# Kernel tuning notes

Measured on AMD Instinct MI355X. Metric: run time of the kernel, lower is better.

The kernel has to match this reference:

```python
import jax, jax.numpy as jnp
import numpy as np

E = 8        # num_experts
K = 2        # experts_per_token
D = 1024     # embed_dim
F = 4096     # expert intermediate (mlp_ratio * D)
FS = 2048    # shared-expert intermediate (n_shared_experts * D)
B, S = 2, 1024


def setup_inputs() -> dict:
    key = jax.random.key(0)
    ks = jax.random.split(key, 8)
    scale = jnp.float32(0.02)
    return {
        "x": jax.random.normal(ks[0], (B, S, D), jnp.float32),
        "gate_w": jax.random.normal(ks[1], (E, D), jnp.float32) * scale,
        "gate_k": jax.random.normal(ks[2], (E, D, F), jnp.float32) * scale,
        "up_k": jax.random.normal(ks[3], (E, D, F), jnp.float32) * scale,
        "down_k": jax.random.normal(ks[4], (E, F, D), jnp.float32) * scale,
        "sh_gate": jax.random.normal(ks[5], (D, FS), jnp.float32) * scale,
        "sh_up": jax.random.normal(ks[6], (D, FS), jnp.float32) * scale,
        "sh_down": jax.random.normal(ks[7], (FS, D), jnp.float32) * scale,
    }


def reference(x, gate_w, gate_k, up_k, down_k, sh_gate, sh_up, sh_down):
    b, s, d = x.shape
    xt = x.reshape(-1, d)                                   # [N, D] tokens

    # --- router gate: softmax over expert logits, then top-k ---
    logits = xt @ gate_w.T                                  # [N, E]
    scores = jax.nn.softmax(logits, axis=-1)
    topk_w, topk_i = jax.lax.top_k(scores, K)               # [N, K] each
    # norm_topk_prob = False -> use raw softmax top-k weights

    # per-token combine weights over experts: [N, E]
    combine = (jax.nn.one_hot(topk_i, E, dtype=xt.dtype) * topk_w[..., None]).sum(axis=1)

    # --- routed experts: SwiGLU MLP per expert (batched over E) ---
    g = jnp.einsum("nd,edf->enf", xt, gate_k)               # [E, N, F]
    u = jnp.einsum("nd,edf->enf", xt, up_k)                 # [E, N, F]
    a = jax.nn.silu(g) * u                                  # [E, N, F]
    eo = jnp.einsum("enf,efd->end", a, down_k)              # [E, N, D]
    y = jnp.einsum("end,ne->nd", eo, combine)               # [N, D]

    # --- shared expert (SwiGLU) on identity input ---
    shared = (jax.nn.silu(xt @ sh_gate) * (xt @ sh_up)) @ sh_down  # [N, D]

    return (y + shared).reshape(b, s, d)
```

## Files before the change

### kernel.cpp

```cpp
#include <hip/hip_runtime.h>
#include <hip/hip_bf16.h>

#define E_ 8
#define K_ 2
#define D_ 1024
#define F_ 4096
#define FS_ 2048
#define N_ 2048
#define ROWS_CAP 4352
#define NCHUNK 8
#define CHUNK_CAP 8

typedef __bf16 bf16x8 __attribute__((ext_vector_type(8)));
typedef float f32x4 __attribute__((ext_vector_type(4)));

static __device__ __forceinline__ unsigned short f2bf(float f) {
  union { float f; unsigned int u; } v; v.f = f;
  unsigned int u = v.u;
  return (unsigned short)((u + 0x7FFF + ((u >> 16) & 1)) >> 16);
}

static __device__ __forceinline__ void gload16(const unsigned short* gp, unsigned short* lp) {
  __builtin_amdgcn_global_load_lds(
      (const __attribute__((address_space(1))) unsigned int*)gp,
      (__attribute__((address_space(3))) unsigned int*)lp, 16, 0, 0);
}

__global__ void init_k(int* counts) {
  if (threadIdx.x < E_) counts[threadIdx.x] = 0;
}

__global__ void router_k(const float* __restrict__ x, const float* __restrict__ gw,
                         unsigned short* __restrict__ xbf, float* __restrict__ topw,
                         int* __restrict__ topi, int* __restrict__ counts) {
  int wave = threadIdx.x >> 6, lane = threadIdx.x & 63;
  int n = blockIdx.x * 4 + wave;
  const float* xr = x + (size_t)n * D_;
  float v[16];
#pragma unroll
  for (int j = 0; j < 16; ++j) v[j] = xr[lane + 64 * j];
#pragma unroll
  for (int j = 0; j < 16; ++j) xbf[(size_t)n * D_ + lane + 64 * j] = f2bf(v[j]);
  float logit[E_];
  for (int e = 0; e < E_; ++e) {
    const float* g = gw + e * D_;
    float acc = 0.f;
#pragma unroll
    for (int j = 0; j < 16; ++j) acc += v[j] * g[lane + 64 * j];
#pragma unroll
    for (int off = 32; off > 0; off >>= 1) acc += __shfl_down(acc, off, 64);
    logit[e] = __shfl(acc, 0, 64);
  }
  if (lane == 0) {
    float m = logit[0];
    for (int e = 1; e < E_; ++e) m = fmaxf(m, logit[e]);
    float p[E_], s = 0.f;
    for (int e = 0; e < E_; ++e) { p[e] = expf(logit[e] - m); s += p[e]; }
    float inv = 1.f / s;
    for (int e = 0; e < E_; ++e) p[e] *= inv;
    int i0 = 0;
    for (int e = 1; e < E_; ++e) if (p[e] > p[i0]) i0 = e;
    int i1 = (i0 == 0) ? 1 : 0;
    for (int e = 0; e < E_; ++e) if (e != i0 && p[e] > p[i1]) i1 = e;
    topi[n * 2] = i0; topi[n * 2 + 1] = i1;
    topw[n * 2] = p[i0]; topw[n * 2 + 1] = p[i1];
    atomicAdd(&counts[i0], 1);
    atomicAdd(&counts[i1], 1);
  }
}

__global__ void scan_k(const int* __restrict__ counts, int* __restrict__ offs,
                       int* __restrict__ cursor, int* __restrict__ tile_e,
                       int* __restrict__ tile_m) {
  if (threadIdx.x == 0) {
    int load[NCHUNK];
    for (int c = 0; c < NCHUNK; ++c) load[c] = 0;
    for (int i = 0; i < NCHUNK * CHUNK_CAP; ++i) tile_e[i] = -1;
    int o = 0;
    for (int e = 0; e < E_; ++e) {
      offs[e] = o;
      int c = counts[e];
      int mt = (c + 127) >> 7;
      int best = 0;
      for (int c2 = 1; c2 < NCHUNK; ++c2) if (load[c2] < load[best]) best = c2;
      for (int m = 0; m < mt; ++m) {
        int ch = best;
        if (load[ch] >= CHUNK_CAP) {
          ch = 0;
          for (int c2 = 1; c2 < NCHUNK; ++c2) if (load[c2] < load[ch]) ch = c2;
        }
        tile_e[ch * CHUNK_CAP + load[ch]] = e;
        tile_m[ch * CHUNK_CAP + load[ch]] = m;
        load[ch]++;
      }
      o += c; cursor[e] = 0;
    }
    offs[E_] = o;
  }
}

__global__ void fill_k(const int* __restrict__ topi, const float* __restrict__ topw,
                       const int* __restrict__ offs,
                       int* __restrict__ cursor, int* __restrict__ rowlist,
                       int* __restrict__ slot_of, float* __restrict__ roww) {
  int n = blockIdx.x * blockDim.x + threadIdx.x;
  if (n >= N_) return;
  for (int k = 0; k < K_; ++k) {
    int e = topi[n * 2 + k];
    int pos = offs[e] + atomicAdd(&cursor[e], 1);
    rowlist[pos] = n;
    slot_of[n * 2 + k] = pos;
    roww[pos] = topw[n * 2 + k];
  }
}

__global__ void transpose_cvt_k(const float* __restrict__ in, unsigned short* __restrict__ out,
                                int R, int C) {
  __shared__ float tile[64][65];
  int cb = blockIdx.x * 64, rb = blockIdx.y * 64;
  const float* ip = in + (size_t)blockIdx.z * R * C;
  unsigned short* op = out + (size_t)blockIdx.z * R * C;
  int t = threadIdx.x;
  int cg = (t & 15) * 4, r0 = t >> 4;
#pragma unroll
  for (int p = 0; p < 4; ++p) {
    int r = r0 + p * 16;
    float4 v = *(const float4*)&ip[(size_t)(rb + r) * C + cb + cg];
    tile[r][cg] = v.x; tile[r][cg + 1] = v.y; tile[r][cg + 2] = v.z; tile[r][cg + 3] = v.w;
  }
  __syncthreads();
  int wx = t & 31, wy = t >> 5;
#pragma unroll
  for (int i = 0; i < 8; ++i) {
    int cl = wy + i * 8;
    unsigned int u = (unsigned int)f2bf(tile[2 * wx][cl]) |
                     ((unsigned int)f2bf(tile[2 * wx + 1][cl]) << 16);
    ((unsigned int*)(op + (size_t)(cb + cl) * R + rb))[wx] = u;
  }
}

#define G1_STAGE(buf, kt2)                               \
    gload16(aptr0 + (kt2) * 32, &As[buf][aoff0]);        \
    gload16(aptr1 + (kt2) * 32, &As[buf][aoff1]);        \
    gload16(bgptr + (kt2) * 32, &Bgs[buf][boff]);        \
    gload16(buptr + (kt2) * 32, &Bus[buf][boff]);

#define G1_STEP(buf, kt)                                                        \
  {                                                                             \
    if ((kt) + 1 < nk) {                                                        \
      G1_STAGE(1 - (buf), (kt) + 1)                                             \
      asm volatile("s_waitcnt vmcnt(4)" ::: "memory");                          \
    } else {                                                                    \
      asm volatile("s_waitcnt vmcnt(0)" ::: "memory");                          \
    }                                                                           \
    __builtin_amdgcn_s_barrier();                                               \
    __builtin_amdgcn_sched_barrier(0);                                          \
    bf16x8 afr[4];                                                              \
    _Pragma("unroll") for (int i = 0; i < 4; ++i)                               \
      afr[i] = *(const bf16x8*)&As[buf][(wm * 64 + i * 16 + (lane & 15)) * 32 + (lane >> 4) * 8]; \
    _Pragma("unroll") for (int j = 0; j < 2; ++j) {                             \
      bf16x8 bg = *(const bf16x8*)&Bgs[buf][(wn * 32 + j * 16 + (lane & 15)) * 32 + (lane >> 4) * 8]; \
      bf16x8 bu = *(const bf16x8*)&Bus[buf][(wn * 32 + j * 16 + (lane & 15)) * 32 + (lane >> 4) * 8]; \
      _Pragma("unroll") for (int i = 0; i < 4; ++i) {                           \
        accg[i][j] = __builtin_amdgcn_mfma_f32_16x16x32_bf16(afr[i], bg, accg[i][j], 0, 0, 0); \
        accu[i][j] = __builtin_amdgcn_mfma_f32_16x16x32_bf16(afr[i], bu, accu[i][j], 0, 0, 0); \
      }                                                                         \
    }                                                                           \
    __builtin_amdgcn_sched_barrier(0);                                          \
    __builtin_amdgcn_s_barrier();                                               \
  }

__launch_bounds__(256, 3)
__global__ void gemm1_k(const unsigned short* __restrict__ Abase,
                        const int* __restrict__ rowlist,
                        const int* __restrict__ offs,
                        const int* __restrict__ tile_e, const int* __restrict__ tile_m,
                        int swz, int Mfixed,
                        const unsigned short* __restrict__ Bg_base,
                        const unsigned short* __restrict__ Bu_base,
                        int Ncols, int Kdim,
                        unsigned short* __restrict__ Out) {
  int e, mbase, Me, slotbase, nbase;
  if (swz) {
    int slot = blockIdx.x * CHUNK_CAP + (blockIdx.y & (CHUNK_CAP - 1));
    e = tile_e[slot];
    if (e < 0) return;
    mbase = tile_m[slot] * 128;
    slotbase = offs[e]; Me = offs[e + 1] - slotbase;
    nbase = (int)(blockIdx.y >> 3) * 64;
  } else {
    e = 0; mbase = blockIdx.x * 128; slotbase = 0; Me = Mfixed;
    nbase = blockIdx.y * 64;
  }
  const unsigned short* Bg = Bg_base + (size_t)e * Ncols * Kdim;
  const unsigned short* Bu = Bu_base + (size_t)e * Ncols * Kdim;

  __shared__ unsigned short As[2][128 * 32];
  __shared__ unsigned short Bgs[2][64 * 32];
  __shared__ unsigned short Bus[2][64 * 32];

  int t = threadIdx.x, lane = t & 63, wave = t >> 6;
  int wm = wave >> 1, wn = wave & 1;
  int chunk = lane & 3, rsub = lane >> 2;

  int g0 = mbase + wave * 32 + rsub;
  int g1 = mbase + wave * 32 + 16 + rsub;
  int src0, src1;
  if (rowlist) {
    src0 = rowlist[slotbase + ((g0 < Me) ? (g0 - mbase) + mbase : 0)];
    src1 = rowlist[slotbase + ((g1 < Me) ? g1 : 0)];
    src0 = rowlist[slotbase + ((g0 < Me) ? g0 : 0)];
  } else {
    src0 = (g0 < Me) ? g0 : 0;
    src1 = (g1 < Me) ? g1 : 0;
  }
  const unsigned short* aptr0 = Abase + (size_t)src0 * Kdim + chunk * 8;
  const unsigned short* aptr1 = Abase + (size_t)src1 * Kdim + chunk * 8;
  unsigned int aoff0 = (unsigned)(wave * 32) * 32;
  unsigned int aoff1 = (unsigned)(wave * 32 + 16) * 32;
  int bn = nbase + wave * 16 + rsub;
  const unsigned short* bgptr = Bg + (size_t)bn * Kdim + chunk * 8;
  const unsigned short* buptr = Bu + (size_t)bn * Kdim + chunk * 8;
  unsigned int boff = (unsigned)(wave * 16) * 32;

  f32x4 accg[4][2], accu[4][2];
#pragma unroll
  for (int i = 0; i < 4; ++i)
#pragma unroll
    for (int j = 0; j < 2; ++j) {
      accg[i][j] = f32x4{0.f, 0.f, 0.f, 0.f};
      accu[i][j] = f32x4{0.f, 0.f, 0.f, 0.f};
    }

  int nk = Kdim >> 5;
  G1_STAGE(0, 0)
  for (int kt = 0; kt < nk; kt += 2) {
    G1_STEP(0, kt)
    G1_STEP(1, kt + 1)
  }

  int r0 = (lane >> 4) * 4, cn = lane & 15;
#pragma unroll
  for (int i = 0; i < 4; ++i) {
#pragma unroll
    for (int rr = 0; rr < 4; ++rr) {
      int grow = mbase + wm * 64 + i * 16 + r0 + rr;
      if (grow < Me) {
        size_t rbase = (size_t)(slotbase + grow) * Ncols + nbase;
#pragma unroll
        for (int j = 0; j < 2; ++j) {
          float g = accg[i][j][rr], u = accu[i][j][rr];
          float a = (g / (1.f + __expf(-g))) * u;
          Out[rbase + wn * 32 + j * 16 + cn] = f2bf(a);
        }
      }
    }
  }
}

#define G2_STAGE(buf, kt2)                               \
    gload16(aptr0 + (kt2) * 32, &As[buf][loff0]);        \
    gload16(aptr1 + (kt2) * 32, &As[buf][loff1]);        \
    gload16(bptr0 + (kt2) * 32, &Bs[buf][loff0]);        \
    gload16(bptr1 + (kt2) * 32, &Bs[buf][loff1]);

#define G2_STEP(buf, kt)                                                        \
  {                                                                             \
    if ((kt) + 1 < nk) {                                                        \
      G2_STAGE(1 - (buf), (kt) + 1)                                             \
      asm volatile("s_waitcnt vmcnt(4)" ::: "memory");                          \
    } else {                                                                    \
      asm volatile("s_waitcnt vmcnt(0)" ::: "memory");                          \
    }                                                                           \
    __builtin_amdgcn_s_barrier();                                               \
    __builtin_amdgcn_sched_barrier(0);                                          \
    bf16x8 afr[4];                                                              \
    _Pragma("unroll") for (int i = 0; i < 4; ++i)                               \
      afr[i] = *(const bf16x8*)&As[buf][(wm * 64 + i * 16 + (lane & 15)) * 32 + (lane >> 4) * 8]; \
    _Pragma("unroll") for (int j = 0; j < 4; ++j) {                             \
      bf16x8 bb = *(const bf16x8*)&Bs[buf][(wn * 64 + j * 16 + (lane & 15)) * 32 + (lane >> 4) * 8]; \
      _Pragma("unroll") for (int i = 0; i < 4; ++i)                             \
        acc[i][j] = __builtin_amdgcn_mfma_f32_16x16x32_bf16(afr[i], bb, acc[i][j], 0, 0, 0); \
    }                                                                           \
    __builtin_amdgcn_sched_barrier(0);                                          \
    __builtin_amdgcn_s_barrier();                                               \
  }

__launch_bounds__(256, 3)
__global__ void gemm2_k(const unsigned short* __restrict__ Abase,
                        const int* __restrict__ rowlist,
                        const float* __restrict__ roww,
                        const int* __restrict__ offs,
                        const int* __restrict__ tile_e, const int* __restrict__ tile_m,
                        int swz, int Mfixed,
                        const unsigned short* __restrict__ Bt_base,
                        int Ncols, int Kdim, int kchunk,
                        float* __restrict__ Out) {
  int e, mbase, Me, slotbase, nbase, koff;
  if (swz) {
    int slot = blockIdx.x * CHUNK_CAP + (blockIdx.y & (CHUNK_CAP - 1));
    e = tile_e[slot];
    if (e < 0) return;
    mbase = tile_m[slot] * 128;
    slotbase = offs[e]; Me = offs[e + 1] - slotbase;
    int r = blockIdx.y >> 3;
    nbase = (r & 7) * 128;
    koff = (r >> 3) * kchunk;
  } else {
    e = 0; mbase = blockIdx.x * 128; slotbase = 0; Me = Mfixed;
    nbase = blockIdx.y * 128;
    koff = blockIdx.z * kchunk;
  }
  const unsigned short* Bt = Bt_base + (size_t)e * Ncols * Kdim;

  __shared__ unsigned short As[2][128 * 32];
  __shared__ unsigned short Bs[2][128 * 32];

  int t = threadIdx.x, lane = t & 63, wave = t >> 6;
  int wm = wave >> 1, wn = wave & 1;
  int chunk = lane & 3, rsub = lane >> 2;

  int ra = wave * 32 + rsub, rb2 = wave * 32 + 16 + rsub;
  int g0 = mbase + ra, g1 = mbase + rb2;
  int arow0 = slotbase + ((g0 < Me) ? g0 : 0);
  int arow1 = slotbase + ((g1 < Me) ? g1 : 0);
  const unsigned short* aptr0 = Abase + (size_t)arow0 * Kdim + koff + chunk * 8;
  const unsigned short* aptr1 = Abase + (size_t)arow1 * Kdim + koff + chunk * 8;
  const unsigned short* bptr0 = Bt + (size_t)(nbase + ra) * Kdim + koff + chunk * 8;
  const unsigned short* bptr1 = Bt + (size_t)(nbase + rb2) * Kdim + koff + chunk * 8;
  unsigned int loff0 = (unsigned)(wave * 32) * 32;
  unsigned int loff1 = (unsigned)(wave * 32 + 16) * 32;

  f32x4 acc[4][4];
#pragma unroll
  for (int i = 0; i < 4; ++i)
#pragma unroll
    for (int j = 0; j < 4; ++j) acc[i][j] = f32x4{0.f, 0.f, 0.f, 0.f};

  int nk = kchunk >> 5;
  G2_STAGE(0, 0)
  for (int kt = 0; kt < nk; kt += 2) {
    G2_STEP(0, kt)
    G2_STEP(1, kt + 1)
  }

  int er0 = (lane >> 4) * 4, cn = lane & 15;
#pragma unroll
  for (int i = 0; i < 4; ++i) {
#pragma unroll
    for (int rr = 0; rr < 4; ++rr) {
      int grow = mbase + wm * 64 + i * 16 + er0 + rr;
      if (grow < Me) {
        int srow = slotbase + grow;
        int token; float wgt;
        if (rowlist) { token = rowlist[srow]; wgt = roww[srow]; }
        else { token = grow; wgt = 1.f; }
        float* orow = Out + (size_t)token * Ncols + nbase + wn * 64 + cn;
#pragma unroll
        for (int j = 0; j < 4; ++j)
          atomicAdd(&orow[j * 16], wgt * acc[i][j][rr]);
      }
    }
  }
}

__launch_bounds__(256, 2)
__global__ void gemm1_old(const unsigned short* __restrict__ Abase,
                          const int* __restrict__ rowlist,
                          const int* __restrict__ offs, int Mfixed,
                          const float* __restrict__ Bg_base,
                          const float* __restrict__ Bu_base,
                          int Ncols, int Kdim,
                          unsigned short* __restrict__ Out) {
  int e = blockIdx.z;
  int Me, slotbase;
  if (offs) { slotbase = offs[e]; Me = offs[e + 1] - slotbase; }
  else      { slotbase = 0;       Me = Mfixed; }
  int mbase = blockIdx.x * 128;
  if (mbase >= Me) return;
  int nbase = blockIdx.y * 128;
  const float* Bg = Bg_base + (size_t)e * Kdim * Ncols;
  const float* Bu = Bu_base + (size_t)e * Kdim * Ncols;
  __shared__ unsigned short As[128][40];
  __shared__ unsigned short Bgs[128][40];
  __shared__ unsigned short Bus[128][40];
  int t = threadIdx.x, lane = t & 63, wave = t >> 6;
  int wm = wave >> 1, wn = wave & 1;
  f32x4 accg[4][4], accu[4][4];
#pragma unroll
  for (int i = 0; i < 4; ++i)
#pragma unroll
    for (int j = 0; j < 4; ++j) {
      accg[i][j] = f32x4{0.f, 0.f, 0.f, 0.f};
      accu[i][j] = f32x4{0.f, 0.f, 0.f, 0.f};
    }
  int ar = t >> 1, akh = t & 1;
  int arow = mbase + ar;
  int asrc = 0;
  if (arow < Me) asrc = rowlist ? rowlist[slotbase + arow] : arow;
  const unsigned short* aptr = Abase + (size_t)asrc * Kdim + akh * 16;
  int bfc = t & 127, bkh = t >> 7;
  const float* bgp = Bg + (size_t)(bkh * 16) * Ncols + nbase + bfc;
  const float* bup = Bu + (size_t)(bkh * 16) * Ncols + nbase + bfc;
  int nk = Kdim >> 5;
  for (int kt = 0; kt < nk; ++kt) {
    uint4 a0 = *(const uint4*)(aptr + kt * 32);
    uint4 a1 = *(const uint4*)(aptr + kt * 32 + 8);
    *(uint4*)&As[ar][akh * 16] = a0;
    *(uint4*)&As[ar][akh * 16 + 8] = a1;
    {
      const float* p0 = bgp + (size_t)kt * 32 * Ncols;
      float bv[16]; unsigned short h[16];
#pragma unroll
      for (int i = 0; i < 16; ++i) bv[i] = p0[(size_t)i * Ncols];
#pragma unroll
      for (int i = 0; i < 16; ++i) h[i] = f2bf(bv[i]);
      *(uint4*)&Bgs[bfc][bkh * 16] = *(uint4*)&h[0];
      *(uint4*)&Bgs[bfc][bkh * 16 + 8] = *(uint4*)&h[8];
    }
    {
      const float* p1 = bup + (size_t)kt * 32 * Ncols;
      float bv[16]; unsigned short h[16];
#pragma unroll
      for (int i = 0; i < 16; ++i) bv[i] = p1[(size_t)i * Ncols];
#pragma unroll
      for (int i = 0; i < 16; ++i) h[i] = f2bf(bv[i]);
      *(uint4*)&Bus[bfc][bkh * 16] = *(uint4*)&h[0];
      *(uint4*)&Bus[bfc][bkh * 16 + 8] = *(uint4*)&h[8];
    }
    __syncthreads();
    bf16x8 afr[4];
#pragma unroll
    for (int i = 0; i < 4; ++i)
      afr[i] = *(const bf16x8*)&As[wm * 64 + i * 16 + (lane & 15)][(lane >> 4) * 8];
#pragma unroll
    for (int j = 0; j < 4; ++j) {
      bf16x8 bg = *(const bf16x8*)&Bgs[wn * 64 + j * 16 + (lane & 15)][(lane >> 4) * 8];
      bf16x8 bu = *(const bf16x8*)&Bus[wn * 64 + j * 16 + (lane & 15)][(lane >> 4) * 8];
#pragma unroll
      for (int i = 0; i < 4; ++i) {
        accg[i][j] = __builtin_amdgcn_mfma_f32_16x16x32_bf16(afr[i], bg, accg[i][j], 0, 0, 0);
        accu[i][j] = __builtin_amdgcn_mfma_f32_16x16x32_bf16(afr[i], bu, accu[i][j], 0, 0, 0);
      }
    }
    __syncthreads();
  }
  int r0 = (lane >> 4) * 4, cn = lane & 15;
#pragma unroll
  for (int i = 0; i < 4; ++i) {
#pragma unroll
    for (int rr = 0; rr < 4; ++rr) {
      int grow = mbase + wm * 64 + i * 16 + r0 + rr;
      if (grow < Me) {
        size_t rbase = (size_t)(slotbase + grow) * Ncols + nbase;
#pragma unroll
        for (int j = 0; j < 4; ++j) {
          float g = accg[i][j][rr], u = accu[i][j][rr];
          float a = (g / (1.f + __expf(-g))) * u;
          Out[rbase + wn * 64 + j * 16 + cn] = f2bf(a);
        }
      }
    }
  }
}

__launch_bounds__(256, 2)
__global__ void gemm2_old(const unsigned short* __restrict__ Abase,
                          const int* __restrict__ offs, int Mfixed,
                          const float* __restrict__ B_base,
                          int Ncols, int Kdim,
                          float* __restrict__ Out) {
  int e = blockIdx.z;
  int Me, slotbase;
  if (offs) { slotbase = offs[e]; Me = offs[e + 1] - slotbase; }
  else      { slotbase = 0;       Me = Mfixed; }
  int mbase = blockIdx.x * 128;
  if (mbase >= Me) return;
  int nbase = blockIdx.y * 128;
  const float* B = B_base + (size_t)e * Kdim * Ncols;
  __shared__ unsigned short As[128][40];
  __shared__ unsigned short Bs[128][40];
  int t = threadIdx.x, lane = t & 63, wave = t >> 6;
  int wm = wave >> 1, wn = wave & 1;
  f32x4 acc[4][4];
#pragma unroll
  for (int i = 0; i < 4; ++i)
#pragma unroll
    for (int j = 0; j < 4; ++j) acc[i][j] = f32x4{0.f, 0.f, 0.f, 0.f};
  int ar = t >> 1, akh = t & 1;
  int arow = slotbase + ((mbase + ar < Me) ? (mbase + ar) : 0);
  const unsigned short* aptr = Abase + (size_t)arow * Kdim + akh * 16;
  int bfc = t & 127, bkh = t >> 7;
  const float* bp = B + (size_t)(bkh * 16) * Ncols + nbase + bfc;
  int nk = Kdim >> 5;
  for (int kt = 0; kt < nk; ++kt) {
    uint4 a0 = *(const uint4*)(aptr + kt * 32);
    uint4 a1 = *(const uint4*)(aptr + kt * 32 + 8);
    *(uint4*)&As[ar][akh * 16] = a0;
    *(uint4*)&As[ar][akh * 16 + 8] = a1;
    {
      const float* p0 = bp + (size_t)kt * 32 * Ncols;
      float bv[16]; unsigned short h[16];
#pragma unroll
      for (int i = 0; i < 16; ++i) bv[i] = p0[(size_t)i * Ncols];
#pragma unroll
      for (int i = 0; i < 16; ++i) h[i] = f2bf(bv[i]);
      *(uint4*)&Bs[bfc][bkh * 16] = *(uint4*)&h[0];
      *(uint4*)&Bs[bfc][bkh * 16 + 8] = *(uint4*)&h[8];
    }
    __syncthreads();
    bf16x8 afr[4];
#pragma unroll
    for (int i = 0; i < 4; ++i)
      afr[i] = *(const bf16x8*)&As[wm * 64 + i * 16 + (lane & 15)][(lane >> 4) * 8];
#pragma unroll
    for (int j = 0; j < 4; ++j) {
      bf16x8 bb = *(const bf16x8*)&Bs[wn * 64 + j * 16 + (lane & 15)][(lane >> 4) * 8];
#pragma unroll
      for (int i = 0; i < 4; ++i)
        acc[i][j] = __builtin_amdgcn_mfma_f32_16x16x32_bf16(afr[i], bb, acc[i][j], 0, 0, 0);
    }
    __syncthreads();
  }
  int r0 = (lane >> 4) * 4, cn = lane & 15;
#pragma unroll
  for (int i = 0; i < 4; ++i) {
#pragma unroll
    for (int rr = 0; rr < 4; ++rr) {
      int grow = mbase + wm * 64 + i * 16 + r0 + rr;
      if (grow < Me) {
        size_t rbase = (size_t)(slotbase + grow) * Ncols + nbase;
#pragma unroll
        for (int j = 0; j < 4; ++j)
          Out[rbase + wn * 64 + j * 16 + cn] = acc[i][j][rr];
      }
    }
  }
}

__global__ void combine_k(const float* __restrict__ eo, const float* __restrict__ sh,
                          const float* __restrict__ topw, const int* __restrict__ slot_of,
                          float* __restrict__ out) {
  int idx = blockIdx.x * blockDim.x + threadIdx.x;
  int n = idx >> 8;
  int d4 = idx & 255;
  float w0 = topw[n * 2], w1 = topw[n * 2 + 1];
  int s0 = slot_of[n * 2], s1 = slot_of[n * 2 + 1];
  float4 a = ((const float4*)(eo + (size_t)s0 * D_))[d4];
  float4 b = ((const float4*)(eo + (size_t)s1 * D_))[d4];
  float4 c = ((const float4*)(sh + (size_t)n * D_))[d4];
  float4 r;
  r.x = w0 * a.x + w1 * b.x + c.x;
  r.y = w0 * a.y + w1 * b.y + c.y;
  r.z = w0 * a.z + w1 * b.z + c.z;
  r.w = w0 * a.w + w1 * b.w + c.w;
  ((float4*)out)[idx] = r;
}

extern "C" void kernel_launch(void* const* d_in, const int* in_sizes, int n_in,
                              void* d_out, int out_size, void* d_ws, size_t ws_size,
                              hipStream_t stream) {
  const float* x  = (const float*)d_in[0];
  const float* gw = (const float*)d_in[1];
  const float* gk = (const float*)d_in[2];
  const float* uk = (const float*)d_in[3];
  const float* dk = (const float*)d_in[4];
  const float* sg = (const float*)d_in[5];
  const float* su = (const float*)d_in[6];
  const float* sd = (const float*)d_in[7];
  float* out = (float*)d_out;

  char* w = (char*)d_ws;
  size_t o = 0;
  auto take = [&](size_t bytes) -> void* {
    void* p = w + o;
    o += (bytes + 255) & ~(size_t)255;
    return p;
  };
  unsigned short* xbf    = (unsigned short*)take((size_t)N_ * D_ * 2);
  unsigned short* act    = (unsigned short*)take((size_t)ROWS_CAP * F_ * 2);
  unsigned short* act_sh = (unsigned short*)take((size_t)N_ * FS_ * 2);
  float* eo     = (float*)take((size_t)ROWS_CAP * D_ * 4);
  float* sh_out = (float*)take((size_t)N_ * D_ * 4);
  float* topw   = (float*)take((size_t)N_ * 2 * 4);
  int* topi     = (int*)take((size_t)N_ * 2 * 4);
  int* slot_of  = (int*)take((size_t)N_ * 2 * 4);
  int* rowlist  = (int*)take((size_t)ROWS_CAP * 4);
  int* counts   = (int*)take(E_ * 4);
  int* offs     = (int*)take((E_ + 1) * 4);
  int* cursor   = (int*)take(E_ * 4);
  int* tile_e   = (int*)take(NCHUNK * CHUNK_CAP * 4);
  int* tile_m   = (int*)take(NCHUNK * CHUNK_CAP * 4);
  float* roww = eo;
  unsigned short* gkt = (unsigned short*)take((size_t)E_ * D_ * F_ * 2);
  unsigned short* ukt = (unsigned short*)take((size_t)E_ * D_ * F_ * 2);
  unsigned short* dkt = (unsigned short*)take((size_t)E_ * D_ * F_ * 2);
  unsigned short* sgt = (unsigned short*)take((size_t)D_ * FS_ * 2);
  unsigned short* sut = (unsigned short*)take((size_t)D_ * FS_ * 2);
  unsigned short* sdt = (unsigned short*)take((size_t)D_ * FS_ * 2);
  bool full = (ws_size >= o);

  hipLaunchKernelGGL(init_k, dim3(1), dim3(64), 0, stream, counts);
  hipLaunchKernelGGL(router_k, dim3(N_ / 4), dim3(256), 0, stream,
                     x, gw, xbf, topw, topi, counts);
  hipLaunchKernelGGL(scan_k, dim3(1), dim3(32), 0, stream,
                     counts, offs, cursor, tile_e, tile_m);
  hipLaunchKernelGGL(fill_k, dim3(N_ / 256), dim3(256), 0, stream,
                     topi, topw, offs, cursor, rowlist, slot_of, roww);

  if (full) {
    hipLaunchKernelGGL(transpose_cvt_k, dim3(F_ / 64, D_ / 64, E_), dim3(256), 0, stream,
                       gk, gkt, D_, F_);
    hipLaunchKernelGGL(transpose_cvt_k, dim3(F_ / 64, D_ / 64, E_), dim3(256), 0, stream,
                       uk, ukt, D_, F_);
    hipLaunchKernelGGL(transpose_cvt_k, dim3(D_ / 64, F_ / 64, E_), dim3(256), 0, stream,
                       dk, dkt, F_, D_);
    hipLaunchKernelGGL(transpose_cvt_k, dim3(FS_ / 64, D_ / 64, 1), dim3(256), 0, stream,
                       sg, sgt, D_, FS_);
    hipLaunchKernelGGL(transpose_cvt_k, dim3(FS_ / 64, D_ / 64, 1), dim3(256), 0, stream,
                       su, sut, D_, FS_);
    hipLaunchKernelGGL(transpose_cvt_k, dim3(D_ / 64, FS_ / 64, 1), dim3(256), 0, stream,
                       sd, sdt, FS_, D_);
    hipMemsetAsync(out, 0, (size_t)N_ * D_ * 4, stream);
    hipLaunchKernelGGL(gemm1_k, dim3(NCHUNK, CHUNK_CAP * (F_ / 64)), dim3(256), 0, stream,
                       xbf, rowlist, offs, tile_e, tile_m, 1, 0,
                       gkt, ukt, F_, D_, act);
    hipLaunchKernelGGL(gemm1_k, dim3(N_ / 128, FS_ / 64), dim3(256), 0, stream,
                       xbf, (const int*)nullptr, (const int*)nullptr,
                       (const int*)nullptr, (const int*)nullptr, 0, N_,
                       sgt, sut, FS_, D_, act_sh);
    hipLaunchKernelGGL(gemm2_k, dim3(NCHUNK, CHUNK_CAP * (D_ / 128) * 2), dim3(256), 0, stream,
                       act, rowlist, roww, offs, tile_e, tile_m, 1, 0,
                       dkt, D_, F_, F_ / 2, out);
    hipLaunchKernelGGL(gemm2_k, dim3(N_ / 128, D_ / 128, 2), dim3(256), 0, stream,
                       act_sh, (const int*)nullptr, (const float*)nullptr,
                       (const int*)nullptr, (const int*)nullptr, (const int*)nullptr, 0, N_,
                       sdt, D_, FS_, FS_ / 2, out);
  } else {
    hipLaunchKernelGGL(gemm1_old, dim3(16, F_ / 128, E_), dim3(256), 0, stream,
                       xbf, rowlist, offs, 0, gk, uk, F_, D_, act);
    hipLaunchKernelGGL(gemm1_old, dim3(16, FS_ / 128, 1), dim3(256), 0, stream,
                       xbf, (const int*)nullptr, (const int*)nullptr, N_, sg, su, FS_, D_, act_sh);
    hipLaunchKernelGGL(gemm2_old, dim3(16, D_ / 128, E_), dim3(256), 0, stream,
                       act, offs, 0, dk, D_, F_, eo);
    hipLaunchKernelGGL(gemm2_old, dim3(16, D_ / 128, 1), dim3(256), 0, stream,
                       act_sh, (const int*)nullptr, N_, sd, D_, FS_, sh_out);
    hipLaunchKernelGGL(combine_k, dim3((N_ * D_ / 4) / 256), dim3(256), 0, stream,
                       eo, sh_out, topw, slot_of, out);
  }
}
```

Measured before the change: 794.9 us.

## Use chunk-major LDS tile layout and simplify double-buffer synchronization in MoE GEMMs

Both grouped GEMM kernels change their LDS tile layout so each 16-row slab is stored chunk-major. The lanes of an MFMA operand read then hit contiguous LDS addresses, which removes the strided row accesses that caused bank conflicts. The hand-written vmcnt waits and split barriers are replaced by a prefetch-next, compute-current, __syncthreads loop, and a redundant rowlist load is removed. The trade-off is that each barrier now waits for the prefetch just issued, which may reduce how much of the global-load latency is hidden.

```diff
diff --git a/kernel.cpp b/kernel.cpp
--- a/kernel.cpp
+++ b/kernel.cpp
@@ -145,29 +145,19 @@
     gload16(bgptr + (kt2) * 32, &Bgs[buf][boff]);        \
     gload16(buptr + (kt2) * 32, &Bus[buf][boff]);
 
-#define G1_STEP(buf, kt)                                                        \
+#define G1_COMPUTE(buf)                                                         \
   {                                                                             \
-    if ((kt) + 1 < nk) {                                                        \
-      G1_STAGE(1 - (buf), (kt) + 1)                                             \
-      asm volatile("s_waitcnt vmcnt(4)" ::: "memory");                          \
-    } else {                                                                    \
-      asm volatile("s_waitcnt vmcnt(0)" ::: "memory");                          \
-    }                                                                           \
-    __builtin_amdgcn_s_barrier();                                               \
-    __builtin_amdgcn_sched_barrier(0);                                          \
     bf16x8 afr[4];                                                              \
     _Pragma("unroll") for (int i = 0; i < 4; ++i)                               \
-      afr[i] = *(const bf16x8*)&As[buf][(wm * 64 + i * 16 + (lane & 15)) * 32 + (lane >> 4) * 8]; \
+      afr[i] = *(const bf16x8*)&As[buf][(wm * 4 + i) * 512 + chunk * 128 + rsub * 8]; \
     _Pragma("unroll") for (int j = 0; j < 2; ++j) {                             \
-      bf16x8 bg = *(const bf16x8*)&Bgs[buf][(wn * 32 + j * 16 + (lane & 15)) * 32 + (lane >> 4) * 8]; \
-      bf16x8 bu = *(const bf16x8*)&Bus[buf][(wn * 32 + j * 16 + (lane & 15)) * 32 + (lane >> 4) * 8]; \
+      bf16x8 bg = *(const bf16x8*)&Bgs[buf][(wn * 2 + j) * 512 + chunk * 128 + rsub * 8]; \
+      bf16x8 bu = *(const bf16x8*)&Bus[buf][(wn * 2 + j) * 512 + chunk * 128 + rsub * 8]; \
       _Pragma("unroll") for (int i = 0; i < 4; ++i) {                           \
         accg[i][j] = __builtin_amdgcn_mfma_f32_16x16x32_bf16(afr[i], bg, accg[i][j], 0, 0, 0); \
         accu[i][j] = __builtin_amdgcn_mfma_f32_16x16x32_bf16(afr[i], bu, accu[i][j], 0, 0, 0); \
       }                                                                         \
     }                                                                           \
-    __builtin_amdgcn_sched_barrier(0);                                          \
-    __builtin_amdgcn_s_barrier();                                               \
   }
 
 __launch_bounds__(256, 3)
@@ -201,27 +191,26 @@
 
   int t = threadIdx.x, lane = t & 63, wave = t >> 6;
   int wm = wave >> 1, wn = wave & 1;
-  int chunk = lane & 3, rsub = lane >> 2;
+  int chunk = lane >> 4, rsub = lane & 15;
 
   int g0 = mbase + wave * 32 + rsub;
-  int g1 = mbase + wave * 32 + 16 + rsub;
+  int g1 = g0 + 16;
   int src0, src1;
   if (rowlist) {
-    src0 = rowlist[slotbase + ((g0 < Me) ? (g0 - mbase) + mbase : 0)];
+    src0 = rowlist[slotbase + ((g0 < Me) ? g0 : 0)];
     src1 = rowlist[slotbase + ((g1 < Me) ? g1 : 0)];
-    src0 = rowlist[slotbase + ((g0 < Me) ? g0 : 0)];
   } else {
     src0 = (g0 < Me) ? g0 : 0;
     src1 = (g1 < Me) ? g1 : 0;
   }
   const unsigned short* aptr0 = Abase + (size_t)src0 * Kdim + chunk * 8;
   const unsigned short* aptr1 = Abase + (size_t)src1 * Kdim + chunk * 8;
-  unsigned int aoff0 = (unsigned)(wave * 32) * 32;
-  unsigned int aoff1 = (unsigned)(wave * 32 + 16) * 32;
+  unsigned int aoff0 = (unsigned)(wave * 2) * 512;
+  unsigned int aoff1 = aoff0 + 512;
   int bn = nbase + wave * 16 + rsub;
   const unsigned short* bgptr = Bg + (size_t)bn * Kdim + chunk * 8;
   const unsigned short* buptr = Bu + (size_t)bn * Kdim + chunk * 8;
-  unsigned int boff = (unsigned)(wave * 16) * 32;
+  unsigned int boff = (unsigned)wave * 512;
 
   f32x4 accg[4][2], accu[4][2];
 #pragma unroll
@@ -234,9 +223,14 @@
 
   int nk = Kdim >> 5;
   G1_STAGE(0, 0)
+  __syncthreads();
   for (int kt = 0; kt < nk; kt += 2) {
-    G1_STEP(0, kt)
-    G1_STEP(1, kt + 1)
+    if (kt + 1 < nk) { G1_STAGE(1, kt + 1) }
+    G1_COMPUTE(0)
+    __syncthreads();
+    if (kt + 2 < nk) { G1_STAGE(0, kt + 2) }
+    G1_COMPUTE(1)
+    __syncthreads();
   }
 
   int r0 = (lane >> 4) * 4, cn = lane & 15;
@@ -264,26 +258,16 @@
     gload16(bptr0 + (kt2) * 32, &Bs[buf][loff0]);        \
     gload16(bptr1 + (kt2) * 32, &Bs[buf][loff1]);
 
-#define G2_STEP(buf, kt)                                                        \
+#define G2_COMPUTE(buf)                                                         \
   {                                                                             \
-    if ((kt) + 1 < nk) {                                                        \
-      G2_STAGE(1 - (buf), (kt) + 1)                                             \
-      asm volatile("s_waitcnt vmcnt(4)" ::: "memory");                          \
-    } else {                                                                    \
-      asm volatile("s_waitcnt vmcnt(0)" ::: "memory");                          \
-    }                                                                           \
-    __builtin_amdgcn_s_barrier();                                               \
-    __builtin_amdgcn_sched_barrier(0);                                          \
     bf16x8 afr[4];                                                              \
     _Pragma("unroll") for (int i = 0; i < 4; ++i)                               \
-      afr[i] = *(const bf16x8*)&As[buf][(wm * 64 + i * 16 + (lane & 15)) * 32 + (lane >> 4) * 8]; \
+      afr[i] = *(const bf16x8*)&As[buf][(wm * 4 + i) * 512 + chunk * 128 + rsub * 8]; \
     _Pragma("unroll") for (int j = 0; j < 4; ++j) {                             \
-      bf16x8 bb = *(const bf16x8*)&Bs[buf][(wn * 64 + j * 16 + (lane & 15)) * 32 + (lane >> 4) * 8]; \
+      bf16x8 bb = *(const bf16x8*)&Bs[buf][(wn * 4 + j) * 512 + chunk * 128 + rsub * 8]; \
       _Pragma("unroll") for (int i = 0; i < 4; ++i)                             \
         acc[i][j] = __builtin_amdgcn_mfma_f32_16x16x32_bf16(afr[i], bb, acc[i][j], 0, 0, 0); \
     }                                                                           \
-    __builtin_amdgcn_sched_barrier(0);                                          \
-    __builtin_amdgcn_s_barrier();                                               \
   }
 
 __launch_bounds__(256, 3)
@@ -318,9 +302,9 @@
 
   int t = threadIdx.x, lane = t & 63, wave = t >> 6;
   int wm = wave >> 1, wn = wave & 1;
-  int chunk = lane & 3, rsub = lane >> 2;
-
-  int ra = wave * 32 + rsub, rb2 = wave * 32 + 16 + rsub;
+  int chunk = lane >> 4, rsub = lane & 15;
+
+  int ra = wave * 32 + rsub, rb2 = ra + 16;
   int g0 = mbase + ra, g1 = mbase + rb2;
   int arow0 = slotbase + ((g0 < Me) ? g0 : 0);
   int arow1 = slotbase + ((g1 < Me) ? g1 : 0);
@@ -328,8 +312,8 @@
   const unsigned short* aptr1 = Abase + (size_t)arow1 * Kdim + koff + chunk * 8;
   const unsigned short* bptr0 = Bt + (size_t)(nbase + ra) * Kdim + koff + chunk * 8;
   const unsigned short* bptr1 = Bt + (size_t)(nbase + rb2) * Kdim + koff + chunk * 8;
-  unsigned int loff0 = (unsigned)(wave * 32) * 32;
-  unsigned int loff1 = (unsigned)(wave * 32 + 16) * 32;
+  unsigned int loff0 = (unsigned)(wave * 2) * 512;
+  unsigned int loff1 = loff0 + 512;
 
   f32x4 acc[4][4];
 #pragma unroll
@@ -339,9 +323,14 @@
 
   int nk = kchunk >> 5;
   G2_STAGE(0, 0)
+  __syncthreads();
   for (int kt = 0; kt < nk; kt += 2) {
-    G2_STEP(0, kt)
-    G2_STEP(1, kt + 1)
+    if (kt + 1 < nk) { G2_STAGE(1, kt + 1) }
+    G2_COMPUTE(0)
+    __syncthreads();
+    if (kt + 2 < nk) { G2_STAGE(0, kt + 2) }
+    G2_COMPUTE(1)
+    __syncthreads();
   }
 
   int er0 = (lane >> 4) * 4, cn = lane & 15;
```

After: 942.3 us. 1.19x slower.
